# Kernel tuning notes

Measured on AMD Instinct MI355X. Metric: run time of the kernel, lower is better.

The kernel has to match this reference:

```python
import jax, jax.numpy as jnp
import numpy as np
import math

D_MODEL, NHEAD, D_FF = 1024, 16, 4096
B, S = 8, 1024
D_K = D_MODEL // NHEAD
EPS = 1e-5


def _layer_norm(x, g, b):
    m = jnp.mean(x, axis=-1, keepdims=True)
    v = jnp.mean(jnp.square(x - m), axis=-1, keepdims=True)
    return (x - m) * jax.lax.rsqrt(v + EPS) * g + b


def setup_inputs() -> dict:
    key = jax.random.key(0)
    ks = jax.random.split(key, 12)
    w = 0.02  # weight scale for numerical sanity
    d, f = D_MODEL, D_FF
    return {
        "x": jax.random.normal(ks[0], (B, S, d), jnp.float32),
        "Wq": jax.random.normal(ks[1], (d, d), jnp.float32) * w, "bq": jnp.zeros((d,), jnp.float32),
        "Wk": jax.random.normal(ks[2], (d, d), jnp.float32) * w, "bk": jnp.zeros((d,), jnp.float32),
        "Wv": jax.random.normal(ks[3], (d, d), jnp.float32) * w, "bv": jnp.zeros((d,), jnp.float32),
        "Wo": jax.random.normal(ks[4], (d, d), jnp.float32) * w, "bo": jnp.zeros((d,), jnp.float32),
        "conv_w": jax.random.normal(ks[5], (d, 3), jnp.float32) * w, "conv_b": jnp.zeros((d,), jnp.float32),
        "lna_g": jnp.ones((d,), jnp.float32), "lna_b": jnp.zeros((d,), jnp.float32),
        "W1": jax.random.normal(ks[6], (d, f), jnp.float32) * w, "b1": jnp.zeros((f,), jnp.float32),
        "W2": jax.random.normal(ks[7], (f, f), jnp.float32) * w, "b2": jnp.zeros((f,), jnp.float32),
        "W3": jax.random.normal(ks[8], (f, d), jnp.float32) * w, "b3": jnp.zeros((d,), jnp.float32),
        "Wg": jax.random.normal(ks[9], (d, d), jnp.float32) * w, "bg": jnp.zeros((d,), jnp.float32),
        "n1_g": jnp.ones((d,), jnp.float32), "n1_b": jnp.zeros((d,), jnp.float32),
        "n2_g": jnp.ones((d,), jnp.float32), "n2_b": jnp.zeros((d,), jnp.float32),
    }


def _forward(x, Wq, bq, Wk, bk, Wv, bv, Wo, bo, conv_w, conv_b, lna_g, lna_b,
             W1, b1, W2, b2, W3, b3, Wg, bg, n1_g, n1_b, n2_g, n2_b):
    b_, s_, d = x.shape
    # --- MultiScaleAttention (eval mode: dropout = identity) ---
    q = (x @ Wq + bq).reshape(b_, s_, NHEAD, D_K).transpose(0, 2, 1, 3)  # [B,H,S,Dk]
    k = (x @ Wk + bk).reshape(b_, s_, NHEAD, D_K).transpose(0, 2, 1, 3)
    v = (x @ Wv + bv).reshape(b_, s_, NHEAD, D_K).transpose(0, 2, 1, 3)
    scores = jnp.einsum('bhqd,bhkd->bhqk', q, k) / math.sqrt(D_K)
    attn = jax.nn.softmax(scores, axis=-1)
    glob = jnp.einsum('bhqk,bhkd->bhqd', attn, v).transpose(0, 2, 1, 3).reshape(b_, s_, d)
    glob = glob @ Wo + bo
    # depthwise conv1d, k=3, pad=1, over seq dim
    xp = jnp.pad(x, ((0, 0), (1, 1), (0, 0)))
    local = (xp[:, :-2] * conv_w[:, 0] + xp[:, 1:-1] * conv_w[:, 1]
             + xp[:, 2:] * conv_w[:, 2] + conv_b)
    attn_out = _layer_norm(x + glob + 0.3 * local, lna_g, lna_b)
    # --- layer body ---
    h = _layer_norm(x + attn_out, n1_g, n1_b)
    ffn = jax.nn.gelu(h @ W1 + b1, approximate=False)
    ffn = jax.nn.gelu(ffn @ W2 + b2, approximate=False)
    ffn = ffn @ W3 + b3
    gate = jax.nn.sigmoid(h @ Wg + bg)
    out = _layer_norm(h + ffn * gate, n2_g, n2_b)
    return out


def reference(x, Wq, bq, Wk, bk, Wv, bv, Wo, bo, conv_w, conv_b, lna_g, lna_b,
              W1, b1, W2, b2, W3, b3, Wg, bg, n1_g, n1_b, n2_g, n2_b):
    return _forward(x, Wq, bq, Wk, bk, Wv, bv, Wo, bo, conv_w, conv_b, lna_g, lna_b,
                    W1, b1, W2, b2, W3, b3, Wg, bg, n1_g, n1_b, n2_g, n2_b)
```

## Files before the change

kernel.cpp:

```cpp
#include <hip/hip_runtime.h>
#include <hip/hip_bf16.h>

typedef unsigned short u16;
typedef __bf16 bf16x8 __attribute__((ext_vector_type(8)));
typedef float floatx4 __attribute__((ext_vector_type(4)));
typedef __attribute__((address_space(3))) const char* lds_cp;

#define MFMA16(a, b, c) __builtin_amdgcn_mfma_f32_16x16x32_bf16((a), (b), (c), 0, 0, 0)

__device__ __forceinline__ u16 f2bf(float f) {
  __bf16 h = (__bf16)f;
  return __builtin_bit_cast(u16, h);
}
__device__ __forceinline__ float bf2f(u16 v) {
  unsigned int u = ((unsigned int)v) << 16;
  return __builtin_bit_cast(float, u);
}

__device__ __forceinline__ void async_copy16(const void* g, void* l) {
  __builtin_amdgcn_global_load_lds(
      (const __attribute__((address_space(1))) unsigned int*)g,
      (__attribute__((address_space(3))) unsigned int*)l, 16, 0, 0);
}

__device__ __forceinline__ bf16x8 ds_read16(lds_cp p) {
  bf16x8 r;
  asm volatile("ds_read_b128 %0, %1" : "=v"(r) : "v"(p));
  return r;
}

__global__ void sentinel_k(float* out, float v) {
  if (threadIdx.x == 0 && blockIdx.x == 0) out[0] = v;
}

__global__ __launch_bounds__(256) void cast_k(const float* __restrict__ in,
                                              u16* __restrict__ out, size_t n) {
  size_t i = ((size_t)blockIdx.x * 256 + threadIdx.x) * 8;
  if (i >= n) return;
  float4 a = *(const float4*)&in[i];
  float4 b = *(const float4*)&in[i + 4];
  union { u16 q[8]; uint4 u; } pk;
  pk.q[0] = f2bf(a.x); pk.q[1] = f2bf(a.y); pk.q[2] = f2bf(a.z); pk.q[3] = f2bf(a.w);
  pk.q[4] = f2bf(b.x); pk.q[5] = f2bf(b.y); pk.q[6] = f2bf(b.z); pk.q[7] = f2bf(b.w);
  *(uint4*)&out[i] = pk.u;
}

__global__ __launch_bounds__(256) void tcast_k(const float* __restrict__ W,
                                               u16* __restrict__ Wt, int K, int N) {
  __shared__ __align__(16) u16 T[64][72];
  const int tid = threadIdx.x;
  const int k0 = blockIdx.x * 64, n0 = blockIdx.y * 64;
  const int r = tid >> 2, cg = (tid & 3) * 16;
#pragma unroll
  for (int j = 0; j < 4; ++j) {
    float4 w = *(const float4*)&W[(size_t)(k0 + r) * N + n0 + cg + j * 4];
    union { u16 q[4]; uint2 u; } pk;
    pk.q[0] = f2bf(w.x); pk.q[1] = f2bf(w.y); pk.q[2] = f2bf(w.z); pk.q[3] = f2bf(w.w);
    *(uint2*)&T[r][cg + j * 4] = pk.u;
  }
  __syncthreads();
  const int n = tid >> 2, kg = (tid & 3) * 16;
#pragma unroll
  for (int j = 0; j < 4; ++j) {
    union { u16 q[4]; uint2 u; } pk;
#pragma unroll
    for (int i = 0; i < 4; ++i) pk.q[i] = T[kg + j * 4 + i][n];
    *(uint2*)&Wt[(size_t)(n0 + n) * K + k0 + kg + j * 4] = pk.u;
  }
}

__global__ __launch_bounds__(256) void catbias_k(const float* __restrict__ a,
                                                 const float* __restrict__ b,
                                                 const float* __restrict__ c,
                                                 float* __restrict__ o) {
  int i = blockIdx.x * 256 + threadIdx.x;
  if (i >= 3072) return;
  o[i] = i < 1024 ? a[i] : (i < 2048 ? b[i - 1024] : c[i - 2048]);
}

__global__ __launch_bounds__(256) void tv_k(const u16* __restrict__ V,
                                            u16* __restrict__ Vt, int VS) {
  __shared__ __align__(16) u16 T[64][72];
  const int bh = blockIdx.x, st = blockIdx.y;
  const int b = bh >> 4, h = bh & 15;
  const int s0 = st * 64;
  const int tid = threadIdx.x;
  const int r = tid >> 2, cg = (tid & 3) * 16;
#pragma unroll
  for (int j = 0; j < 2; ++j) {
    uint4 v = *(const uint4*)&V[(size_t)(b * 1024 + s0 + r) * VS + h * 64 + cg + j * 8];
    *(uint4*)&T[r][cg + j * 8] = v;
  }
  __syncthreads();
  const int dk = tid >> 2, sg = (tid & 3) * 16;
#pragma unroll
  for (int j = 0; j < 2; ++j) {
    union { u16 q[8]; uint4 u; } pk;
#pragma unroll
    for (int i = 0; i < 8; ++i) pk.q[i] = T[sg + j * 8 + i][dk];
    *(uint4*)&Vt[(size_t)(bh * 64 + dk) * 1024 + s0 + sg + j * 8] = pk.u;
  }
}

template <int NF, int ACT, int OBF>
__global__ __launch_bounds__(512, 2) void gemm8_k(const u16* __restrict__ A,
                                                  const u16* __restrict__ Bt,
                                                  const float* __restrict__ bias,
                                                  void* __restrict__ Cout,
                                                  int M, int N, int K, float scale) {
  constexpr int BN = NF * 64;
  constexpr int NIB = NF / 2;
  __shared__ __align__(16) u16 As[2][2][256 * 32];
  __shared__ __align__(16) u16 Bs[2][2][BN * 32];

  const int tid = threadIdx.x;
  const int lane = tid & 63, wv = tid >> 6;
  const int wm = wv >> 2, wn = wv & 3;
  const int g = lane >> 4, li = lane & 15;
  const int m0 = blockIdx.x * 256, n0 = blockIdx.y * BN;
  const int NT = K >> 6;

  const int srow = lane >> 2;
  const int sk8 = (lane & 3) ^ ((srow >> 1) & 3);
  const size_t abase = (size_t)(m0 + wv * 32 + srow) * K + sk8 * 8;
  const size_t bbase = (size_t)(n0 + wv * (16 * NIB) + srow) * K + sk8 * 8;

  auto stA = [&](int tt, int kh, int p) {
#pragma unroll
    for (int j = 0; j < 2; ++j)
      async_copy16(A + abase + (size_t)j * 16 * K + tt * 64 + kh * 32,
                   (char*)&As[p][kh][0] + (wv * 2 + j) * 1024);
  };
  auto stB = [&](int tt, int kh, int p) {
#pragma unroll
    for (int j = 0; j < NIB; ++j)
      async_copy16(Bt + bbase + (size_t)j * 16 * K + tt * 64 + kh * 32,
                   (char*)&Bs[p][kh][0] + (wv * NIB + j) * 1024);
  };
  auto ldA = [&](int mf, int kh, int p) -> bf16x8 {
    int r = wm * 128 + mf * 16 + li;
    int byte = (r * 64 + g * 16) ^ (((li >> 1) & 3) << 4);
    return ds_read16((lds_cp)(const char*)&As[p][kh][0] + byte);
  };
  auto ldB = [&](int nf, int kh, int p) -> bf16x8 {
    int n = wn * (16 * NF) + nf * 16 + li;
    int byte = (n * 64 + g * 16) ^ (((li >> 1) & 3) << 4);
    return ds_read16((lds_cp)(const char*)&Bs[p][kh][0] + byte);
  };

  floatx4 acc[8][NF] = {};

  stB(0, 0, 0); stB(0, 1, 0); stA(0, 0, 0); stA(0, 1, 0);
  stB(1, 0, 1); stB(1, 1, 1); stA(1, 0, 1);
  if constexpr (NF == 4) asm volatile("s_waitcnt vmcnt(6)");
  else                   asm volatile("s_waitcnt vmcnt(4)");
  __builtin_amdgcn_s_barrier();

  for (int t = 0; t < NT; ++t) {
    const int p = t & 1, pn = p ^ 1;
    const int t1 = (t + 1 < NT) ? t + 1 : t + 1 - NT;
    const int t2 = (t + 2 < NT) ? t + 2 : t + 2 - NT;
    bf16x8 a[4], b0[NF], b1[NF];

#pragma unroll
    for (int mf = 0; mf < 4; ++mf) a[mf] = ldA(mf, 0, p);
#pragma unroll
    for (int nf = 0; nf < NF; ++nf) b0[nf] = ldB(nf, 0, p);
    stA(t1, 1, pn);
    __builtin_amdgcn_s_barrier();
    asm volatile("s_waitcnt lgkmcnt(0)");
    __builtin_amdgcn_sched_barrier(0);
    __builtin_amdgcn_s_setprio(1);
#pragma unroll
    for (int mf = 0; mf < 4; ++mf)
#pragma unroll
      for (int nf = 0; nf < NF; ++nf)
        acc[mf][nf] = MFMA16(a[mf], b0[nf], acc[mf][nf]);
    __builtin_amdgcn_s_setprio(0);
    __builtin_amdgcn_s_barrier();

#pragma unroll
    for (int mf = 0; mf < 4; ++mf) a[mf] = ldA(mf, 1, p);
#pragma unroll
    for (int nf = 0; nf < NF; ++nf) b1[nf] = ldB(nf, 1, p);
    stB(t2, 0, p);
    __builtin_amdgcn_s_barrier();
    asm volatile("s_waitcnt lgkmcnt(0)");
    __builtin_amdgcn_sched_barrier(0);
    __builtin_amdgcn_s_setprio(1);
#pragma unroll
    for (int mf = 0; mf < 4; ++mf)
#pragma unroll
      for (int nf = 0; nf < NF; ++nf)
        acc[mf][nf] = MFMA16(a[mf], b1[nf], acc[mf][nf]);
    __builtin_amdgcn_s_setprio(0);
    __builtin_amdgcn_s_barrier();

#pragma unroll
    for (int mf = 0; mf < 4; ++mf) a[mf] = ldA(4 + mf, 0, p);
    stB(t2, 1, p);
    __builtin_amdgcn_s_barrier();
    asm volatile("s_waitcnt lgkmcnt(0)");
    __builtin_amdgcn_sched_barrier(0);
    __builtin_amdgcn_s_setprio(1);
#pragma unroll
    for (int mf = 0; mf < 4; ++mf)
#pragma unroll
      for (int nf = 0; nf < NF; ++nf)
        acc[4 + mf][nf] = MFMA16(a[mf], b0[nf], acc[4 + mf][nf]);
    __builtin_amdgcn_s_setprio(0);
    __builtin_amdgcn_s_barrier();

#pragma unroll
    for (int mf = 0; mf < 4; ++mf) a[mf] = ldA(4 + mf, 1, p);
    stA(t2, 0, p);
    if constexpr (NF == 4) asm volatile("s_waitcnt vmcnt(6)");
    else                   asm volatile("s_waitcnt vmcnt(4)");
    __builtin_amdgcn_s_barrier();
    asm volatile("s_waitcnt lgkmcnt(0)");
    __builtin_amdgcn_sched_barrier(0);
    __builtin_amdgcn_s_setprio(1);
#pragma unroll
    for (int mf = 0; mf < 4; ++mf)
#pragma unroll
      for (int nf = 0; nf < NF; ++nf)
        acc[4 + mf][nf] = MFMA16(a[mf], b1[nf], acc[4 + mf][nf]);
    __builtin_amdgcn_s_setprio(0);
    __builtin_amdgcn_s_barrier();
  }
  asm volatile("s_waitcnt vmcnt(0)");

  float bv[NF];
#pragma unroll
  for (int nf = 0; nf < NF; ++nf) bv[nf] = bias[n0 + wn * (16 * NF) + nf * 16 + li];
#pragma unroll
  for (int mf = 0; mf < 8; ++mf)
#pragma unroll
    for (int nf = 0; nf < NF; ++nf)
#pragma unroll
      for (int i = 0; i < 4; ++i) {
        size_t r = (size_t)m0 + wm * 128 + mf * 16 + g * 4 + i;
        size_t c = (size_t)n0 + wn * (16 * NF) + nf * 16 + li;
        float v = (acc[mf][nf][i] + bv[nf]) * scale;
        if (ACT == 1) v = 0.5f * v * (1.0f + erff(v * 0.70710678118654752f));
        if (ACT == 2) v = 1.0f / (1.0f + __expf(-v));
        if (OBF)
          ((u16*)Cout)[r * N + c] = f2bf(v);
        else
          ((float*)Cout)[r * N + c] = v;
      }
}

template <int ACT, int OBF>
__global__ __launch_bounds__(256) void gemm_k(const u16* __restrict__ A,
                                              const u16* __restrict__ Bt,
                                              const float* __restrict__ bias,
                                              void* __restrict__ Cout, int M, int N,
                                              int K, float scale) {
  __shared__ __align__(16) u16 As[128 * 64];
  __shared__ __align__(16) u16 Bs[128 * 64];
  const int tid = threadIdx.x;
  const int lane = tid & 63;
  const int wv = tid >> 6;
  const int m0 = blockIdx.x * 128, n0 = blockIdx.y * 128;
  const int wm = (wv >> 1) * 64, wn = (wv & 1) * 64;

  floatx4 acc[4][4] = {};
  const u16* Ab = A + (size_t)m0 * K;
  const u16* Bb = Bt + (size_t)n0 * K;

  int a_off[4][2], b_off[4][2];
#pragma unroll
  for (int f = 0; f < 4; ++f) {
#pragma unroll
    for (int ks = 0; ks < 2; ++ks) {
      int kk = ks * 32 + ((lane >> 4) << 3);
      int ra = wm + f * 16 + (lane & 15);
      a_off[f][ks] = (ra * 128 + kk * 2) ^ ((ra & 7) << 4);
      int rb = wn + f * 16 + (lane & 15);
      b_off[f][ks] = (rb * 128 + kk * 2) ^ ((rb & 7) << 4);
    }
  }

  for (int kt = 0; kt < K; kt += 64) {
    __syncthreads();
#pragma unroll
    for (int it = 0; it < 4; ++it) {
      int d = it * 256 + tid;
      int row = d >> 3;
      int cgrp = ((d & 7) ^ (row & 7)) << 3;
      async_copy16(Ab + (size_t)row * K + kt + cgrp, (char*)As + (it * 256 + wv * 64) * 16);
      async_copy16(Bb + (size_t)row * K + kt + cgrp, (char*)Bs + (it * 256 + wv * 64) * 16);
    }
    __syncthreads();

    bf16x8 af[4][2], bfr[4][2];
#pragma unroll
    for (int f = 0; f < 4; ++f) {
      af[f][0] = *(const bf16x8*)((const char*)As + a_off[f][0]);
      af[f][1] = *(const bf16x8*)((const char*)As + a_off[f][1]);
      bfr[f][0] = *(const bf16x8*)((const char*)Bs + b_off[f][0]);
      bfr[f][1] = *(const bf16x8*)((const char*)Bs + b_off[f][1]);
    }
#pragma unroll
    for (int mi = 0; mi < 4; ++mi) {
#pragma unroll
      for (int ni = 0; ni < 4; ++ni) {
        acc[mi][ni] = MFMA16(af[mi][0], bfr[ni][0], acc[mi][ni]);
        acc[mi][ni] = MFMA16(af[mi][1], bfr[ni][1], acc[mi][ni]);
      }
    }
  }

  float bv[4];
#pragma unroll
  for (int ni = 0; ni < 4; ++ni) bv[ni] = bias[n0 + wn + ni * 16 + (lane & 15)];
#pragma unroll
  for (int mi = 0; mi < 4; ++mi) {
#pragma unroll
    for (int ni = 0; ni < 4; ++ni) {
#pragma unroll
      for (int i = 0; i < 4; ++i) {
        size_t r = (size_t)m0 + wm + mi * 16 + ((lane >> 4) << 2) + i;
        size_t c = (size_t)n0 + wn + ni * 16 + (lane & 15);
        float v = (acc[mi][ni][i] + bv[ni]) * scale;
        if (ACT == 1) v = 0.5f * v * (1.0f + erff(v * 0.70710678118654752f));
        if (ACT == 2) v = 1.0f / (1.0f + __expf(-v));
        if (OBF)
          ((u16*)Cout)[r * N + c] = f2bf(v);
        else
          ((float*)Cout)[r * N + c] = v;
      }
    }
  }
}

__global__ __launch_bounds__(256) void attn_k(const u16* __restrict__ Q,
                                              const u16* __restrict__ Kb,
                                              const u16* __restrict__ Vt,
                                              u16* __restrict__ Ob, int QS) {
  __shared__ __align__(16) u16 Ks[2][64 * 64];
  __shared__ __align__(16) u16 Vs[2][64 * 64];
  __shared__ __align__(16) u16 Pl[4][2048];
  const int qt = blockIdx.x, bh = blockIdx.y;
  const int b = bh >> 4, h = bh & 15;
  const int tid = threadIdx.x;
  const int lane = tid & 63, wv = tid >> 6;
  const int g = lane >> 4, li = lane & 15;
  const float SC = 0.125f * 1.4426950408889634f;

  bf16x8 qf[2][2];
#pragma unroll
  for (int m = 0; m < 2; ++m) {
    int qrow = qt * 128 + wv * 32 + m * 16 + li;
    const u16* qp = Q + ((size_t)(b * 1024 + qrow)) * QS + h * 64 + g * 8;
    qf[m][0] = *(const bf16x8*)qp;
    qf[m][1] = *(const bf16x8*)(qp + 32);
  }

  float l_i[2][4] = {};
  floatx4 o[2][4] = {};

  const int r0 = tid >> 3;
  const int csrc = ((tid & 7) ^ (r0 & 7)) * 8;
  const u16* Kg = Kb + ((size_t)b * 1024) * QS + h * 64;
  const u16* Vg = Vt + ((size_t)bh * 64) * 1024;
  char* Pw = (char*)&Pl[wv][0];

  auto stage = [&](int bi, int kv0) {
#pragma unroll
    for (int it = 0; it < 2; ++it) {
      int row = it * 32 + r0;
      async_copy16(Kg + (size_t)(kv0 + row) * QS + csrc, &Ks[bi][(it * 256 + wv * 64) * 8]);
      async_copy16(Vg + (size_t)row * 1024 + kv0 + csrc, &Vs[bi][(it * 256 + wv * 64) * 8]);
    }
  };

  stage(0, 0);
  __syncthreads();
  int buf = 0;

  for (int t = 0; t < 16; ++t) {
    if (t < 15) stage(buf ^ 1, (t + 1) * 64);
    const char* kb = (const char*)&Ks[buf][0];
    const char* vb = (const char*)&Vs[buf][0];

    floatx4 s[2][4];
    __builtin_amdgcn_s_setprio(1);
#pragma unroll
    for (int m = 0; m < 2; ++m)
#pragma unroll
      for (int n = 0; n < 4; ++n) {
        int krow = n * 16 + li;
        int by0 = (krow * 128 + g * 16) ^ ((krow & 7) << 4);
        int by1 = (krow * 128 + 64 + g * 16) ^ ((krow & 7) << 4);
        floatx4 z = {0.f, 0.f, 0.f, 0.f};
        s[m][n] = MFMA16(qf[m][0], *(const bf16x8*)(kb + by0), z);
        s[m][n] = MFMA16(qf[m][1], *(const bf16x8*)(kb + by1), s[m][n]);
      }
    __builtin_amdgcn_s_setprio(0);

#pragma unroll
    for (int m = 0; m < 2; ++m) {
      float rs[4] = {0.f, 0.f, 0.f, 0.f};
#pragma unroll
      for (int n = 0; n < 4; ++n)
#pragma unroll
        for (int i = 0; i < 4; ++i) {
          float p = exp2f(s[m][n][i] * SC);
          rs[i] += p;
          int row = m * 16 + g * 4 + i, col = n * 16 + li;
          int byte = (row * 128 + col * 2) ^ ((row & 7) << 4);
          *(u16*)(Pw + byte) = f2bf(p);
        }
#pragma unroll
      for (int off = 8; off >= 1; off >>= 1)
#pragma unroll
        for (int i = 0; i < 4; ++i) rs[i] += __shfl_xor(rs[i], off);
#pragma unroll
      for (int i = 0; i < 4; ++i) l_i[m][i] += rs[i];
    }

    __builtin_amdgcn_s_setprio(1);
#pragma unroll
    for (int m = 0; m < 2; ++m) {
      int prow = m * 16 + li;
      int pb0 = (prow * 128 + g * 16) ^ ((prow & 7) << 4);
      int pb1 = (prow * 128 + 64 + g * 16) ^ ((prow & 7) << 4);
      bf16x8 pf0 = *(const bf16x8*)(Pw + pb0);
      bf16x8 pf1 = *(const bf16x8*)(Pw + pb1);
#pragma unroll
      for (int nd = 0; nd < 4; ++nd) {
        int vrow = nd * 16 + li;
        int vb0 = (vrow * 128 + g * 16) ^ ((vrow & 7) << 4);
        int vb1 = (vrow * 128 + 64 + g * 16) ^ ((vrow & 7) << 4);
        o[m][nd] = MFMA16(pf0, *(const bf16x8*)(vb + vb0), o[m][nd]);
        o[m][nd] = MFMA16(pf1, *(const bf16x8*)(vb + vb1), o[m][nd]);
      }
    }
    __builtin_amdgcn_s_setprio(0);

    __syncthreads();
    buf ^= 1;
  }

#pragma unroll
  for (int m = 0; m < 2; ++m)
#pragma unroll
    for (int nd = 0; nd < 4; ++nd)
#pragma unroll
      for (int i = 0; i < 4; ++i) {
        size_t r = (size_t)(b * 1024 + qt * 128 + wv * 32 + m * 16 + g * 4 + i);
        Ob[r * 1024 + h * 64 + nd * 16 + li] = f2bf(o[m][nd][i] / l_i[m][i]);
      }
}

__device__ __forceinline__ void bsum2(float& a, float& b, float* sred, int tid) {
#pragma unroll
  for (int off = 32; off; off >>= 1) {
    a += __shfl_down(a, off);
    b += __shfl_down(b, off);
  }
  const int wv = tid >> 6;
  if ((tid & 63) == 0) { sred[wv] = a; sred[4 + wv] = b; }
  __syncthreads();
  a = sred[0] + sred[1] + sred[2] + sred[3];
  b = sred[4] + sred[5] + sred[6] + sred[7];
  __syncthreads();
}

__device__ __forceinline__ void ld4(const float* p, float v[4]) {
  float4 t = *(const float4*)p;
  v[0] = t.x; v[1] = t.y; v[2] = t.z; v[3] = t.w;
}
__device__ __forceinline__ void ld4bf(const u16* p, float v[4]) {
  union { uint2 u; u16 q[4]; } t;
  t.u = *(const uint2*)p;
#pragma unroll
  for (int j = 0; j < 4; ++j) v[j] = bf2f(t.q[j]);
}

__global__ __launch_bounds__(256) void post_attn_k(
    const float* __restrict__ x, const u16* __restrict__ G,
    const float* __restrict__ cw, const float* __restrict__ cb,
    const float* __restrict__ lag, const float* __restrict__ lab,
    const float* __restrict__ n1g, const float* __restrict__ n1b,
    u16* __restrict__ hb) {
  __shared__ float sred[8];
  const size_t row = blockIdx.x;
  const int s = (int)(row & 1023);
  const int tid = threadIdx.x, d = tid * 4;

  float xv[4], xm[4] = {0, 0, 0, 0}, xp[4] = {0, 0, 0, 0}, gv[4], cbv[4];
  ld4(&x[row * 1024 + d], xv);
  if (s > 0) ld4(&x[(row - 1) * 1024 + d], xm);
  if (s < 1023) ld4(&x[(row + 1) * 1024 + d], xp);
  ld4bf(&G[row * 1024 + d], gv);
  float c0[4], c1[4], c2[4];
  ld4(&cw[d * 3], c0);
  ld4(&cw[d * 3 + 4], c1);
  ld4(&cw[d * 3 + 8], c2);
  ld4(&cb[d], cbv);
  float w0[4] = {c0[0], c0[3], c1[2], c2[1]};
  float w1[4] = {c0[1], c1[0], c1[3], c2[2]};
  float w2[4] = {c0[2], c1[1], c2[0], c2[3]};

  float t[4], sa = 0.f, sb = 0.f;
#pragma unroll
  for (int j = 0; j < 4; ++j) {
    float loc = xm[j] * w0[j] + xv[j] * w1[j] + xp[j] * w2[j] + cbv[j];
    t[j] = xv[j] + gv[j] + 0.3f * loc;
    sa += t[j];
    sb += t[j] * t[j];
  }
  bsum2(sa, sb, sred, tid);
  float mean = sa * (1.f / 1024.f);
  float rstd = rsqrtf(sb * (1.f / 1024.f) - mean * mean + 1e-5f);
  float lg[4], lbv[4];
  ld4(&lag[d], lg);
  ld4(&lab[d], lbv);
  float hp[4];
  sa = 0.f; sb = 0.f;
#pragma unroll
  for (int j = 0; j < 4; ++j) {
    float a = (t[j] - mean) * rstd * lg[j] + lbv[j];
    hp[j] = xv[j] + a;
    sa += hp[j];
    sb += hp[j] * hp[j];
  }
  bsum2(sa, sb, sred, tid);
  float mean2 = sa * (1.f / 1024.f);
  float rstd2 = rsqrtf(sb * (1.f / 1024.f) - mean2 * mean2 + 1e-5f);
  float g2[4], b2[4];
  ld4(&n1g[d], g2);
  ld4(&n1b[d], b2);
  union { u16 q[4]; uint2 u; } pk;
#pragma unroll
  for (int j = 0; j < 4; ++j) pk.q[j] = f2bf((hp[j] - mean2) * rstd2 * g2[j] + b2[j]);
  *(uint2*)&hb[row * 1024 + d] = pk.u;
}

__global__ __launch_bounds__(256) void final_k(const u16* __restrict__ h,
                                               const u16* __restrict__ f3,
                                               const u16* __restrict__ gt,
                                               const float* __restrict__ n2g,
                                               const float* __restrict__ n2b,
                                               float* __restrict__ out) {
  __shared__ float sred[8];
  const size_t row = blockIdx.x;
  const int tid = threadIdx.x, d = tid * 4;
  float hv[4], fv[4], gv[4];
  ld4bf(&h[row * 1024 + d], hv);
  ld4bf(&f3[row * 1024 + d], fv);
  ld4bf(&gt[row * 1024 + d], gv);
  float t[4], sa = 0.f, sb = 0.f;
#pragma unroll
  for (int j = 0; j < 4; ++j) {
    t[j] = hv[j] + fv[j] * gv[j];
    sa += t[j];
    sb += t[j] * t[j];
  }
  bsum2(sa, sb, sred, tid);
  float mean = sa * (1.f / 1024.f);
  float rstd = rsqrtf(sb * (1.f / 1024.f) - mean * mean + 1e-5f);
  float g2[4], b2[4];
  ld4(&n2g[d], g2);
  ld4(&n2b[d], b2);
  float o[4];
#pragma unroll
  for (int j = 0; j < 4; ++j) o[j] = (t[j] - mean) * rstd * g2[j] + b2[j];
  *(float4*)&out[row * 1024 + d] = make_float4(o[0], o[1], o[2], o[3]);
}

extern "C" void kernel_launch(void* const* d_in, const int* in_sizes, int n_in,
                              void* d_out, int out_size, void* d_ws, size_t ws_size,
                              hipStream_t stream) {
  (void)in_sizes; (void)n_in; (void)out_size;
  const float* x   = (const float*)d_in[0];
  const float* Wq  = (const float*)d_in[1];
  const float* bq  = (const float*)d_in[2];
  const float* Wk  = (const float*)d_in[3];
  const float* bk  = (const float*)d_in[4];
  const float* Wv  = (const float*)d_in[5];
  const float* bv  = (const float*)d_in[6];
  const float* Wo  = (const float*)d_in[7];
  const float* bo  = (const float*)d_in[8];
  const float* cw  = (const float*)d_in[9];
  const float* cb  = (const float*)d_in[10];
  const float* lag = (const float*)d_in[11];
  const float* lab = (const float*)d_in[12];
  const float* W1  = (const float*)d_in[13];
  const float* b1  = (const float*)d_in[14];
  const float* W2  = (const float*)d_in[15];
  const float* b2  = (const float*)d_in[16];
  const float* W3  = (const float*)d_in[17];
  const float* b3  = (const float*)d_in[18];
  const float* Wg  = (const float*)d_in[19];
  const float* bg  = (const float*)d_in[20];
  const float* n1g = (const float*)d_in[21];
  const float* n1b = (const float*)d_in[22];
  const float* n2g = (const float*)d_in[23];
  const float* n2b = (const float*)d_in[24];

  const size_t MB = 1024ull * 1024ull;
  if (ws_size < 122 * MB) {
    sentinel_k<<<1, 64, 0, stream>>>((float*)d_out, (float)ws_size);
    return;
  }
  char* ws = (char*)d_ws;
  char* dob = (char*)d_out;
  u16* WoT   = (u16*)(ws + 0 * MB);
  u16* WgT   = (u16*)(ws + 2 * MB);
  u16* W1T   = (u16*)(ws + 4 * MB);
  u16* W2T   = (u16*)(ws + 12 * MB);
  u16* W3T   = (u16*)(ws + 44 * MB);
  u16* WqkvT = (u16*)(ws + 52 * MB);
  float* bqkv = (float*)(dob + 28 * MB);
  u16* xb    = (u16*)(ws + 58 * MB);
  u16* QKV   = (u16*)(ws + 74 * MB);
  u16* hb    = (u16*)(ws + 74 * MB);
  u16* f1h   = (u16*)(ws + 90 * MB);
  u16* gate  = (u16*)(ws + 90 * MB);
  u16* G     = xb;
  u16* f3    = xb;
  u16* Vt    = (u16*)dob;
  u16* globb = (u16*)(dob + 16 * MB);
  u16* f2h   = (u16*)dob;

  cast_k<<<4096, 256, 0, stream>>>(x, xb, (size_t)8192 * 1024);
  tcast_k<<<dim3(16, 16), 256, 0, stream>>>(Wq, WqkvT, 1024, 1024);
  tcast_k<<<dim3(16, 16), 256, 0, stream>>>(Wk, WqkvT + 1024 * 1024, 1024, 1024);
  tcast_k<<<dim3(16, 16), 256, 0, stream>>>(Wv, WqkvT + 2048 * 1024, 1024, 1024);
  tcast_k<<<dim3(16, 16), 256, 0, stream>>>(Wo, WoT, 1024, 1024);
  tcast_k<<<dim3(16, 16), 256, 0, stream>>>(Wg, WgT, 1024, 1024);
  tcast_k<<<dim3(16, 64), 256, 0, stream>>>(W1, W1T, 1024, 4096);
  tcast_k<<<dim3(64, 64), 256, 0, stream>>>(W2, W2T, 4096, 4096);
  tcast_k<<<dim3(64, 16), 256, 0, stream>>>(W3, W3T, 4096, 1024);
  catbias_k<<<12, 256, 0, stream>>>(bq, bk, bv, bqkv);

  gemm8_k<4, 0, 1><<<dim3(32, 12), 512, 0, stream>>>(xb, WqkvT, bqkv, QKV, 8192, 3072, 1024, 1.0f);
  tv_k<<<dim3(128, 16), 256, 0, stream>>>(QKV + 2048, Vt, 3072);
  attn_k<<<dim3(8, 128), 256, 0, stream>>>(QKV, QKV + 1024, Vt, globb, 3072);
  gemm_k<0, 1><<<dim3(64, 8), 256, 0, stream>>>(globb, WoT, bo, G, 8192, 1024, 1024, 1.0f);
  post_attn_k<<<8192, 256, 0, stream>>>(x, G, cw, cb, lag, lab, n1g, n1b, hb);

  for (int hf = 0; hf < 2; ++hf) {
    const size_t M0 = (size_t)hf * 4096;
    gemm8_k<4, 1, 1><<<dim3(16, 16), 512, 0, stream>>>(hb + M0 * 1024, W1T, b1, f1h,
                                                       4096, 4096, 1024, 1.0f);
    gemm8_k<4, 1, 1><<<dim3(16, 16), 512, 0, stream>>>(f1h, W2T, b2, f2h,
                                                       4096, 4096, 4096, 1.0f);
    gemm_k<0, 1><<<dim3(32, 8), 256, 0, stream>>>(f2h, W3T, b3, f3 + M0 * 1024,
                                                  4096, 1024, 4096, 1.0f);
  }
  gemm_k<2, 1><<<dim3(64, 8), 256, 0, stream>>>(hb, WgT, bg, gate, 8192, 1024, 1024, 1.0f);
  final_k<<<8192, 256, 0, stream>>>(hb, f3, gate, n2g, n2b, (float*)d_out);
}
```

Baseline: 815.1 us.

## Overlap attention K/V prefetch with compute and batch weight transpose launches

The attention loop now waits only for the current buffer's async copies (vmcnt-based) before a raw barrier, instead of a full syncthreads after staging. K, V and P fragments are preloaded into registers with explicit LDS reads before the MFMA blocks, separated by sched barriers. Five 1024x1024 weight transpose-cast launches are merged into one kernel indexed by blockIdx.z to cut launch overhead. The hand-written waitcnt counts depend on the exact number of outstanding async copies per stage.

```diff
diff --git a/kernel.cpp b/kernel.cpp
--- a/kernel.cpp
+++ b/kernel.cpp
@@ -45,11 +45,11 @@
   *(uint4*)&out[i] = pk.u;
 }
 
-__global__ __launch_bounds__(256) void tcast_k(const float* __restrict__ W,
-                                               u16* __restrict__ Wt, int K, int N) {
+__device__ __forceinline__ void tcast_body(const float* __restrict__ W,
+                                           u16* __restrict__ Wt, int K, int N,
+                                           int bx, int by, int tid) {
   __shared__ __align__(16) u16 T[64][72];
-  const int tid = threadIdx.x;
-  const int k0 = blockIdx.x * 64, n0 = blockIdx.y * 64;
+  const int k0 = bx * 64, n0 = by * 64;
   const int r = tid >> 2, cg = (tid & 3) * 16;
 #pragma unroll
   for (int j = 0; j < 4; ++j) {
@@ -67,6 +67,28 @@
     for (int i = 0; i < 4; ++i) pk.q[i] = T[kg + j * 4 + i][n];
     *(uint2*)&Wt[(size_t)(n0 + n) * K + k0 + kg + j * 4] = pk.u;
   }
+}
+
+__global__ __launch_bounds__(256) void tcast_k(const float* __restrict__ W,
+                                               u16* __restrict__ Wt, int K, int N) {
+  tcast_body(W, Wt, K, N, blockIdx.x, blockIdx.y, threadIdx.x);
+}
+
+__global__ __launch_bounds__(256) void tcast5_k(
+    const float* __restrict__ s0, const float* __restrict__ s1,
+    const float* __restrict__ s2, const float* __restrict__ s3,
+    const float* __restrict__ s4, u16* __restrict__ d0, u16* __restrict__ d1,
+    u16* __restrict__ d2, u16* __restrict__ d3, u16* __restrict__ d4) {
+  const float* W;
+  u16* Wt;
+  switch (blockIdx.z) {
+    case 0: W = s0; Wt = d0; break;
+    case 1: W = s1; Wt = d1; break;
+    case 2: W = s2; Wt = d2; break;
+    case 3: W = s3; Wt = d3; break;
+    default: W = s4; Wt = d4; break;
+  }
+  tcast_body(W, Wt, 1024, 1024, blockIdx.x, blockIdx.y, threadIdx.x);
 }
 
 __global__ __launch_bounds__(256) void catbias_k(const float* __restrict__ a,
@@ -377,26 +399,40 @@
   };
 
   stage(0, 0);
-  __syncthreads();
   int buf = 0;
 
   for (int t = 0; t < 16; ++t) {
-    if (t < 15) stage(buf ^ 1, (t + 1) * 64);
+    if (t < 15) {
+      stage(buf ^ 1, (t + 1) * 64);
+      asm volatile("s_waitcnt vmcnt(4)");
+    } else {
+      asm volatile("s_waitcnt vmcnt(0)");
+    }
+    __builtin_amdgcn_s_barrier();
+
     const char* kb = (const char*)&Ks[buf][0];
     const char* vb = (const char*)&Vs[buf][0];
 
+    bf16x8 kf[4][2];
+#pragma unroll
+    for (int n = 0; n < 4; ++n) {
+      int krow = n * 16 + li;
+      int by0 = (krow * 128 + g * 16) ^ ((krow & 7) << 4);
+      int by1 = (krow * 128 + 64 + g * 16) ^ ((krow & 7) << 4);
+      kf[n][0] = ds_read16((lds_cp)kb + by0);
+      kf[n][1] = ds_read16((lds_cp)kb + by1);
+    }
+    asm volatile("s_waitcnt lgkmcnt(0)");
+    __builtin_amdgcn_sched_barrier(0);
     floatx4 s[2][4];
     __builtin_amdgcn_s_setprio(1);
 #pragma unroll
     for (int m = 0; m < 2; ++m)
 #pragma unroll
       for (int n = 0; n < 4; ++n) {
-        int krow = n * 16 + li;
-        int by0 = (krow * 128 + g * 16) ^ ((krow & 7) << 4);
-        int by1 = (krow * 128 + 64 + g * 16) ^ ((krow & 7) << 4);
         floatx4 z = {0.f, 0.f, 0.f, 0.f};
-        s[m][n] = MFMA16(qf[m][0], *(const bf16x8*)(kb + by0), z);
-        s[m][n] = MFMA16(qf[m][1], *(const bf16x8*)(kb + by1), s[m][n]);
+        s[m][n] = MFMA16(qf[m][0], kf[n][0], z);
+        s[m][n] = MFMA16(qf[m][1], kf[n][1], s[m][n]);
       }
     __builtin_amdgcn_s_setprio(0);
 
@@ -421,26 +457,37 @@
       for (int i = 0; i < 4; ++i) l_i[m][i] += rs[i];
     }
 
-    __builtin_amdgcn_s_setprio(1);
+    bf16x8 vf[4][2];
+#pragma unroll
+    for (int nd = 0; nd < 4; ++nd) {
+      int vrow = nd * 16 + li;
+      int vb0 = (vrow * 128 + g * 16) ^ ((vrow & 7) << 4);
+      int vb1 = (vrow * 128 + 64 + g * 16) ^ ((vrow & 7) << 4);
+      vf[nd][0] = ds_read16((lds_cp)vb + vb0);
+      vf[nd][1] = ds_read16((lds_cp)vb + vb1);
+    }
+    bf16x8 pf[2][2];
 #pragma unroll
     for (int m = 0; m < 2; ++m) {
       int prow = m * 16 + li;
       int pb0 = (prow * 128 + g * 16) ^ ((prow & 7) << 4);
       int pb1 = (prow * 128 + 64 + g * 16) ^ ((prow & 7) << 4);
-      bf16x8 pf0 = *(const bf16x8*)(Pw + pb0);
-      bf16x8 pf1 = *(const bf16x8*)(Pw + pb1);
+      pf[m][0] = *(const bf16x8*)(Pw + pb0);
+      pf[m][1] = *(const bf16x8*)(Pw + pb1);
+    }
+    asm volatile("s_waitcnt lgkmcnt(0)");
+    __builtin_amdgcn_sched_barrier(0);
+    __builtin_amdgcn_s_setprio(1);
+#pragma unroll
+    for (int m = 0; m < 2; ++m)
 #pragma unroll
       for (int nd = 0; nd < 4; ++nd) {
-        int vrow = nd * 16 + li;
-        int vb0 = (vrow * 128 + g * 16) ^ ((vrow & 7) << 4);
-        int vb1 = (vrow * 128 + 64 + g * 16) ^ ((vrow & 7) << 4);
-        o[m][nd] = MFMA16(pf0, *(const bf16x8*)(vb + vb0), o[m][nd]);
-        o[m][nd] = MFMA16(pf1, *(const bf16x8*)(vb + vb1), o[m][nd]);
+        o[m][nd] = MFMA16(pf[m][0], vf[nd][0], o[m][nd]);
+        o[m][nd] = MFMA16(pf[m][1], vf[nd][1], o[m][nd]);
       }
-    }
     __builtin_amdgcn_s_setprio(0);
 
-    __syncthreads();
+    __builtin_amdgcn_s_barrier();
     buf ^= 1;
   }
 
@@ -628,11 +675,9 @@
   u16* f2h   = (u16*)dob;
 
   cast_k<<<4096, 256, 0, stream>>>(x, xb, (size_t)8192 * 1024);
-  tcast_k<<<dim3(16, 16), 256, 0, stream>>>(Wq, WqkvT, 1024, 1024);
-  tcast_k<<<dim3(16, 16), 256, 0, stream>>>(Wk, WqkvT + 1024 * 1024, 1024, 1024);
-  tcast_k<<<dim3(16, 16), 256, 0, stream>>>(Wv, WqkvT + 2048 * 1024, 1024, 1024);
-  tcast_k<<<dim3(16, 16), 256, 0, stream>>>(Wo, WoT, 1024, 1024);
-  tcast_k<<<dim3(16, 16), 256, 0, stream>>>(Wg, WgT, 1024, 1024);
+  tcast5_k<<<dim3(16, 16, 5), 256, 0, stream>>>(Wq, Wk, Wv, Wo, Wg,
+                                                WqkvT, WqkvT + 1024 * 1024,
+                                                WqkvT + 2048 * 1024, WoT, WgT);
   tcast_k<<<dim3(16, 64), 256, 0, stream>>>(W1, W1T, 1024, 4096);
   tcast_k<<<dim3(64, 64), 256, 0, stream>>>(W2, W2T, 4096, 4096);
   tcast_k<<<dim3(64, 16), 256, 0, stream>>>(W3, W3T, 4096, 1024);
```

Measured after the change: 814.1 us. No clear change (-0.1%).
